# Optimization experiments

Hardware: AMD Instinct MI355X
Metric: run time of the kernel (lower is better)

The kernel has to match this reference:

```python
import jax, jax.numpy as jnp
import numpy as np

B, N, D = 8, 2048, 128
NEG = -9.0e15


def setup_inputs() -> dict:
    key = jax.random.key(0)
    ks = jax.random.split(key, 7)
    x = jax.random.normal(ks[0], (B, N, D), dtype=jnp.float32)
    # sparse-ish binary adjacency with self loops, stored dense as float
    adj = (jax.random.uniform(ks[1], (B, N, N)) < 0.1).astype(jnp.float32)
    adj = jnp.maximum(adj, jnp.eye(N, dtype=jnp.float32)[None])
    s = 1.0 / np.sqrt(D)
    W_w = jax.random.uniform(ks[2], (D, D), minval=-s, maxval=s, dtype=jnp.float32)
    W_b = jax.random.uniform(ks[3], (D,), minval=-s, maxval=s, dtype=jnp.float32)
    A = jnp.zeros((D, D), dtype=jnp.float32) + 0.01 * jax.random.normal(ks[4], (D, D), dtype=jnp.float32)
    s2 = 1.0 / np.sqrt(2 * D)
    gate_w = jax.random.uniform(ks[5], (1, 2 * D), minval=-s2, maxval=s2, dtype=jnp.float32)
    gate_b = jax.random.uniform(ks[6], (1,), minval=-s2, maxval=s2, dtype=jnp.float32)
    return {"x": x, "adj": adj, "W_w": W_w, "W_b": W_b, "A": A,
            "gate_w": gate_w, "gate_b": gate_b}


def reference(x, adj, W_w, W_b, A, gate_w, gate_b):
    # h = W(x): [B,N,D]
    h = jnp.einsum('bnf,df->bnd', x, W_w) + W_b
    # e[b,j,k] = (h A)[b,j,:] . h[b,k,:], then symmetrize
    hA = jnp.einsum('bnd,de->bne', h, A)
    e = jnp.einsum('bjl,bkl->bjk', hA, h)
    e = e + jnp.swapaxes(e, 1, 2)
    att = jnp.where(adj > 0, e, jnp.full_like(e, NEG))
    # NOTE: torch code softmaxes over dim=1 (the j axis)
    att = jax.nn.softmax(att, axis=1)
    att = att * adj
    h_prime = jax.nn.relu(jnp.einsum('bij,bjk->bik', att, h))
    gate_in = jnp.concatenate([x, h_prime], axis=-1)  # [B,N,2D]
    coeff = jax.nn.sigmoid(jnp.einsum('bnc,oc->bno', gate_in, gate_w) + gate_b)  # [B,N,1]
    return coeff * x + (1.0 - coeff) * h_prime
```

## Files before the change

kernel.cpp:

```cpp
#include <hip/hip_runtime.h>


#define B_ 8
#define N_ 2048
#define D_ 128

typedef __attribute__((ext_vector_type(8))) short short8;
typedef __attribute__((ext_vector_type(4))) float f32x4;
typedef __attribute__((ext_vector_type(2))) float f32x2;

#define GLL(gp, lp) __builtin_amdgcn_global_load_lds( \
    (__attribute__((address_space(1))) const unsigned int*)(gp), \
    (__attribute__((address_space(3))) unsigned int*)(lp), 16, 0, 0)

#define VMW(N) asm volatile("s_waitcnt vmcnt(" #N ")" ::: "memory")
#define BARRIER() __builtin_amdgcn_s_barrier()

static __device__ __forceinline__ unsigned short f2bf(float f) {
  union { float f; unsigned int u; } v; v.f = f;
  unsigned int r = v.u + 0x7fffu + ((v.u >> 16) & 1u);
  return (unsigned short)(r >> 16);
}
static __device__ __forceinline__ float bf2f(unsigned short u) {
  union { unsigned int u; float f; } v; v.u = ((unsigned int)u) << 16;
  return v.f;
}

#define CAT_OFF  ((size_t)0)
#define VT_OFF   ((size_t)8388608)
#define PUN_OFF  ((size_t)12582912)
#define S_OFF    ((size_t)79691776)
#define WB_OFF   ((size_t)79757312)
#define AT_OFF   ((size_t)79790080)

__global__ __launch_bounds__(256) void k_cvt(const float* __restrict__ W,
                                             const float* __restrict__ A,
                                             unsigned short* __restrict__ Wb1,
                                             unsigned short* __restrict__ Abt) {
  int i = blockIdx.x * 256 + threadIdx.x;
  Wb1[i] = f2bf(W[i]);
  Abt[(i & 127) * 128 + (i >> 7)] = f2bf(A[i]);
}

__global__ __launch_bounds__(256) void k1(const float* __restrict__ x,
                                          const unsigned short* __restrict__ Wb1,
                                          const float* __restrict__ Wbias,
                                          const unsigned short* __restrict__ Abt,
                                          unsigned short* __restrict__ cat) {
  __shared__ unsigned short hsm[4][16][136];
  __shared__ unsigned short hasm[4][16][136];
  const int t = threadIdx.x, w = t >> 6, lane = t & 63;
  const int q = lane >> 4, l15 = lane & 15;
  const size_t r0 = (size_t)blockIdx.x * 64 + w * 16;

  f32x4 acc[8];
#pragma unroll
  for (int dg = 0; dg < 8; dg++) acc[dg] = (f32x4){0.f, 0.f, 0.f, 0.f};
#pragma unroll
  for (int k = 0; k < 4; k++) {
    const float* xp = x + (r0 + l15) * 128 + k * 32 + q * 8;
    f32x4 xa = *(const f32x4*)xp;
    f32x4 xb = *(const f32x4*)(xp + 4);
    short8 af;
#pragma unroll
    for (int e = 0; e < 4; e++) { af[e] = (short)f2bf(xa[e]); af[4 + e] = (short)f2bf(xb[e]); }
#pragma unroll
    for (int dg = 0; dg < 8; dg++) {
      short8 bf = *(const short8*)(Wb1 + (dg * 16 + l15) * 128 + k * 32 + q * 8);
      acc[dg] = __builtin_amdgcn_mfma_f32_16x16x32_bf16(af, bf, acc[dg], 0, 0, 0);
    }
  }
#pragma unroll
  for (int dg = 0; dg < 8; dg++) {
    float bias = Wbias[dg * 16 + l15];
#pragma unroll
    for (int r = 0; r < 4; r++)
      hsm[w][q * 4 + r][dg * 16 + l15] = f2bf(acc[dg][r] + bias);
  }
  __syncthreads();
  f32x4 acc2[8];
#pragma unroll
  for (int dg = 0; dg < 8; dg++) acc2[dg] = (f32x4){0.f, 0.f, 0.f, 0.f};
#pragma unroll
  for (int k = 0; k < 4; k++) {
    short8 af = *(short8*)&hsm[w][l15][k * 32 + q * 8];
#pragma unroll
    for (int dg = 0; dg < 8; dg++) {
      short8 bf = *(const short8*)(Abt + (dg * 16 + l15) * 128 + k * 32 + q * 8);
      acc2[dg] = __builtin_amdgcn_mfma_f32_16x16x32_bf16(af, bf, acc2[dg], 0, 0, 0);
    }
  }
#pragma unroll
  for (int dg = 0; dg < 8; dg++)
#pragma unroll
    for (int r = 0; r < 4; r++)
      hasm[w][q * 4 + r][dg * 16 + l15] = f2bf(acc2[dg][r]);
  __syncthreads();
#pragma unroll
  for (int it = 0; it < 8; it++) {
    int idx = it * 64 + lane;
    int row = idx >> 5, c = idx & 31;
    short8 v = (c < 16) ? *(short8*)&hasm[w][row][c * 8]
                        : *(short8*)&hsm[w][row][(c - 16) * 8];
    *(short8*)(cat + ((r0 + row) << 8) + c * 8) = v;
  }
}

__global__ __launch_bounds__(256, 2) void k2(const unsigned short* __restrict__ cat,
                                             const float* __restrict__ adj,
                                             unsigned short* __restrict__ pun,
                                             float* __restrict__ s_out) {
  __shared__ unsigned short cj[2][64 * 256];
  const int t = threadIdx.x, w = t >> 6, lane = t & 63;
  const int q = lane >> 4, l15 = lane & 15;
  const int b = blockIdx.z;
  const int kbase = blockIdx.x * 128;
  const int j0b = blockIdx.y * 512;
  const size_t bN = (size_t)b * N_;
  const unsigned short* catp = cat + (bN << 8);
  const int kc = kbase + w * 32;
  short8 brg[2][8];
#pragma unroll
  for (int p = 0; p < 2; p++) {
    int krow = kc + 2 * l15 + p;
#pragma unroll
    for (int m = 0; m < 8; m++)
      brg[p][m] = *(const short8*)(catp + (((size_t)krow) << 8) +
                                   ((((m * 4 + q) + 16) & 31) * 8));
  }
  float acc0 = 0.f, acc1 = 0.f;

#define K2_STAGE(tt, bufi) do { \
    const int j0_ = j0b + (tt) * 64; \
    _Pragma("unroll") \
    for (int it = 0; it < 8; it++) { \
      int sI = it * 256 + t; \
      int row = sI >> 5, c = sI & 31; \
      GLL(catp + (((size_t)(j0_ + row)) << 8) + (c ^ (row & 7)) * 8, \
          (char*)cj[bufi] + sI * 16); \
    } } while (0)

#define K2_ADJ(tt, av) do { \
    const int j0_ = j0b + (tt) * 64; \
    _Pragma("unroll") \
    for (int js = 0; js < 4; js++) \
      _Pragma("unroll") \
      for (int r = 0; r < 4; r++) { \
        int jrow = j0_ + js * 16 + q * 4 + r; \
        av[js][r] = *(const f32x2*)(adj + (((size_t)(bN + jrow)) << 11) + kc + 2 * l15); \
      } } while (0)

#define K2_COMPUTE(tt, bufi, av) do { \
    const int j0_ = j0b + (tt) * 64; \
    _Pragma("unroll") \
    for (int jsub = 0; jsub < 4; jsub++) { \
      const int row = jsub * 16 + l15; \
      short8 afr[8]; \
      _Pragma("unroll") \
      for (int m = 0; m < 8; m++) \
        afr[m] = *(short8*)(cj[bufi] + row * 256 + (((m * 4 + q) ^ (l15 & 7)) * 8)); \
      f32x4 e0 = {0.f, 0.f, 0.f, 0.f}, e1 = {0.f, 0.f, 0.f, 0.f}; \
      _Pragma("unroll") \
      for (int m = 0; m < 8; m++) { \
        e0 = __builtin_amdgcn_mfma_f32_16x16x32_bf16(afr[m], brg[0][m], e0, 0, 0, 0); \
        e1 = __builtin_amdgcn_mfma_f32_16x16x32_bf16(afr[m], brg[1][m], e1, 0, 0, 0); \
      } \
      _Pragma("unroll") \
      for (int r = 0; r < 4; r++) { \
        int jrow = j0_ + jsub * 16 + q * 4 + r; \
        float x0 = (av[jsub][r][0] > 0.f) ? __expf(fminf(e0[r], 60.f)) : 0.f; \
        float x1 = (av[jsub][r][1] > 0.f) ? __expf(fminf(e1[r], 60.f)) : 0.f; \
        acc0 += x0; acc1 += x1; \
        unsigned int pk = (unsigned int)f2bf(x0) | ((unsigned int)f2bf(x1) << 16); \
        *(unsigned int*)(pun + ((bN + jrow) << 11) + kc + 2 * l15) = pk; \
      } \
    } } while (0)

  f32x2 avA[4][4], avB[4][4];
  K2_STAGE(0, 0);
  K2_ADJ(0, avA);
#pragma unroll
  for (int tp = 0; tp < 4; tp++) {
    K2_STAGE(2 * tp + 1, 1);
    K2_ADJ(2 * tp + 1, avB);
    VMW(40);
    BARRIER();
    K2_COMPUTE(2 * tp, 0, avA);
    BARRIER();
    if (2 * tp + 2 < 8) {
      K2_STAGE(2 * tp + 2, 0);
      K2_ADJ(2 * tp + 2, avA);
      VMW(40);
    } else {
      VMW(16);
    }
    BARRIER();
    K2_COMPUTE(2 * tp + 1, 1, avB);
    BARRIER();
  }
#undef K2_STAGE
#undef K2_ADJ
#undef K2_COMPUTE

  acc0 += __shfl_xor(acc0, 16, 64); acc0 += __shfl_xor(acc0, 32, 64);
  acc1 += __shfl_xor(acc1, 16, 64); acc1 += __shfl_xor(acc1, 32, 64);
  if (lane < 16) {
    atomicAdd(&s_out[bN + kc + 2 * lane], acc0);
    atomicAdd(&s_out[bN + kc + 2 * lane + 1], acc1);
  }
}

__global__ __launch_bounds__(256) void k1v(const unsigned short* __restrict__ cat,
                                           const float* __restrict__ s,
                                           unsigned short* __restrict__ vt) {
  __shared__ unsigned short tile[64][136];
  __shared__ float rsv[64];
  const int t = threadIdx.x;
  const int b = blockIdx.y;
  const int nbase = blockIdx.x * 64;
  if (t < 64) rsv[t] = 1.f / s[(size_t)b * N_ + nbase + t];
#pragma unroll
  for (int k = 0; k < 4; k++) {
    int sI = t + 256 * k;
    int row = sI >> 4, part = sI & 15;
    *(short8*)&tile[row][part * 8] =
        *(const short8*)(cat + (((size_t)(b * N_ + nbase + row)) << 8) + 128 + part * 8);
  }
  __syncthreads();
#pragma unroll
  for (int k = 0; k < 4; k++) {
    int sI = t + 256 * k;
    int dd = sI >> 3, part = sI & 7;
    unsigned short tmp[8];
#pragma unroll
    for (int j = 0; j < 8; j++) {
      int jj = part * 8 + j;
      tmp[j] = f2bf(bf2f(tile[jj][dd]) * rsv[jj]);
    }
    *(short8*)(vt + (((size_t)(b * 128 + dd)) << 11) + nbase + part * 8) = *(short8*)tmp;
  }
}

__global__ __launch_bounds__(256) void k3(const unsigned short* __restrict__ pun,
                                          const unsigned short* __restrict__ vt,
                                          const float* __restrict__ x,
                                          const float* __restrict__ gw,
                                          const float* __restrict__ gb,
                                          float* __restrict__ out) {
  __shared__ char smem[2][40960];
  const int t = threadIdx.x, w = t >> 6, lane = t & 63;
  const int q = lane >> 4, l15 = lane & 15;
  const int b = blockIdx.y, i0 = blockIdx.x * 32;
  const size_t bN = (size_t)b * N_;

  f32x4 acc[2][2];
#pragma unroll
  for (int ih = 0; ih < 2; ih++)
#pragma unroll
    for (int dh = 0; dh < 2; dh++) acc[ih][dh] = (f32x4){0.f, 0.f, 0.f, 0.f};

#define K3_STAGE(jtv, bufi) do { \
    const int j0_ = (jtv) * 128; \
    _Pragma("unroll") \
    for (int it = 0; it < 10; it++) { \
      int sI = it * 256 + t; \
      const unsigned short* g; \
      if (sI < 512) { \
        int row = sI >> 4, c = sI & 15; \
        g = pun + (((size_t)(bN + i0 + row)) << 11) + j0_ + ((c ^ (row & 7)) * 8); \
      } else { \
        int s2 = sI - 512; \
        int dd = s2 >> 4, c = s2 & 15; \
        g = vt + (((size_t)(b * 128 + dd)) << 11) + j0_ + ((c ^ (dd & 7)) * 8); \
      } \
      GLL(g, smem[bufi] + sI * 16); \
    } } while (0)

#define K3_COMPUTE(bufi) do { \
    unsigned short* pa = (unsigned short*)smem[bufi]; \
    unsigned short* vb = (unsigned short*)(smem[bufi] + 8192); \
    _Pragma("unroll") \
    for (int ks = 0; ks < 4; ks++) { \
      short8 af[2], bf[2]; \
      _Pragma("unroll") \
      for (int ih = 0; ih < 2; ih++) { \
        int m = ih * 16 + l15; \
        af[ih] = *(short8*)(pa + m * 128 + (((ks * 4 + q) ^ (m & 7)) * 8)); \
      } \
      _Pragma("unroll") \
      for (int dh = 0; dh < 2; dh++) { \
        int d = w * 32 + dh * 16 + l15; \
        bf[dh] = *(short8*)(vb + d * 128 + (((ks * 4 + q) ^ (d & 7)) * 8)); \
      } \
      acc[0][0] = __builtin_amdgcn_mfma_f32_16x16x32_bf16(af[0], bf[0], acc[0][0], 0, 0, 0); \
      acc[0][1] = __builtin_amdgcn_mfma_f32_16x16x32_bf16(af[0], bf[1], acc[0][1], 0, 0, 0); \
      acc[1][0] = __builtin_amdgcn_mfma_f32_16x16x32_bf16(af[1], bf[0], acc[1][0], 0, 0, 0); \
      acc[1][1] = __builtin_amdgcn_mfma_f32_16x16x32_bf16(af[1], bf[1], acc[1][1], 0, 0, 0); \
    } } while (0)

  K3_STAGE(0, 0);
  for (int jt = 0; jt < 15; jt++) {
    K3_STAGE(jt + 1, (jt + 1) & 1);
    asm volatile("s_waitcnt vmcnt(10)" ::: "memory");
    BARRIER();
    K3_COMPUTE(jt & 1);
    BARRIER();
  }
  asm volatile("s_waitcnt vmcnt(0)" ::: "memory");
  BARRIER();
  K3_COMPUTE(1);
  __syncthreads();
#undef K3_STAGE
#undef K3_COMPUTE

  float* hs = (float*)smem[0];
  float* co = (float*)(smem[0] + 16896);
#pragma unroll
  for (int ih = 0; ih < 2; ih++)
#pragma unroll
    for (int dh = 0; dh < 2; dh++)
#pragma unroll
      for (int r = 0; r < 4; r++) {
        int row = ih * 16 + q * 4 + r;
        int d = w * 32 + dh * 16 + l15;
        hs[row * 132 + d] = fmaxf(acc[ih][dh][r], 0.f);
      }
  __syncthreads();
  {
    int grow = t >> 3, sub = t & 7;
    const float* xr = x + (((size_t)(bN + i0 + grow)) << 7);
    float z = 0.f;
#pragma unroll
    for (int k = 0; k < 16; k++) {
      int dd = sub + 8 * k;
      z += gw[dd] * xr[dd] + gw[128 + dd] * hs[grow * 132 + dd];
    }
    z += __shfl_xor(z, 1, 64);
    z += __shfl_xor(z, 2, 64);
    z += __shfl_xor(z, 4, 64);
    if (sub == 0) co[grow] = 1.f / (1.f + __expf(-(z + gb[0])));
  }
  __syncthreads();
#pragma unroll
  for (int kk = 0; kk < 4; kk++) {
    int id = kk * 256 + t;
    int row = id >> 5, c4 = id & 31;
    size_t g = (((size_t)(bN + i0 + row)) << 7) + c4 * 4;
    f32x4 xv = *(const f32x4*)(x + g);
    f32x4 hv = *(const f32x4*)(hs + row * 132 + c4 * 4);
    float cf = co[row];
    f32x4 o;
#pragma unroll
    for (int e = 0; e < 4; e++) o[e] = cf * xv[e] + (1.f - cf) * hv[e];
    *(f32x4*)(out + g) = o;
  }
}

extern "C" void kernel_launch(void* const* d_in, const int* in_sizes, int n_in,
                              void* d_out, int out_size, void* d_ws, size_t ws_size,
                              hipStream_t stream) {
  const float* x   = (const float*)d_in[0];
  const float* adj = (const float*)d_in[1];
  const float* Ww  = (const float*)d_in[2];
  const float* Wb  = (const float*)d_in[3];
  const float* A   = (const float*)d_in[4];
  const float* gw  = (const float*)d_in[5];
  const float* gb  = (const float*)d_in[6];
  float* out = (float*)d_out;
  char* ws = (char*)d_ws;

  unsigned short* cat = (unsigned short*)(ws + CAT_OFF);
  unsigned short* vt  = (unsigned short*)(ws + VT_OFF);
  unsigned short* pun = (unsigned short*)(ws + PUN_OFF);
  float* s  = (float*)(ws + S_OFF);
  unsigned short* Wb1 = (unsigned short*)(ws + WB_OFF);
  unsigned short* Abt = (unsigned short*)(ws + AT_OFF);

  hipMemsetAsync(s, 0, (size_t)B_ * N_ * sizeof(float), stream);
  k_cvt<<<64, 256, 0, stream>>>(Ww, A, Wb1, Abt);
  k1<<<(B_ * N_) / 64, 256, 0, stream>>>(x, Wb1, Wb, Abt, cat);
  k2<<<dim3(16, 4, B_), 256, 0, stream>>>(cat, adj, pun, s);
  k1v<<<dim3(N_ / 64, B_), 256, 0, stream>>>(cat, s, vt);
  k3<<<dim3(N_ / 32, B_), 256, 0, stream>>>(pun, vt, x, gw, gb, out);
}
```

Baseline: 266.3 us.

## Stage adjacency tiles into LDS via async global_load_lds with smaller j tiles

```diff
diff --git a/kernel.cpp b/kernel.cpp
--- a/kernel.cpp
+++ b/kernel.cpp
@@ -110,7 +110,8 @@
                                              const float* __restrict__ adj,
                                              unsigned short* __restrict__ pun,
                                              float* __restrict__ s_out) {
-  __shared__ unsigned short cj[2][64 * 256];
+  __shared__ unsigned short cj[2][32 * 256];
+  __shared__ float aj[2][32 * 128];
   const int t = threadIdx.x, w = t >> 6, lane = t & 63;
   const int q = lane >> 4, l15 = lane & 15;
   const int b = blockIdx.z;
@@ -131,29 +132,26 @@
   float acc0 = 0.f, acc1 = 0.f;
 
 #define K2_STAGE(tt, bufi) do { \
-    const int j0_ = j0b + (tt) * 64; \
-    _Pragma("unroll") \
-    for (int it = 0; it < 8; it++) { \
+    const int j0_ = j0b + (tt) * 32; \
+    _Pragma("unroll") \
+    for (int it = 0; it < 4; it++) { \
       int sI = it * 256 + t; \
       int row = sI >> 5, c = sI & 31; \
       GLL(catp + (((size_t)(j0_ + row)) << 8) + (c ^ (row & 7)) * 8, \
           (char*)cj[bufi] + sI * 16); \
+    } \
+    _Pragma("unroll") \
+    for (int it = 0; it < 4; it++) { \
+      int sI = it * 256 + t; \
+      int row = sI >> 5, c = sI & 31; \
+      GLL(adj + (((size_t)(bN + j0_ + row)) << 11) + kbase + ((c ^ (row & 7)) << 2), \
+          (char*)aj[bufi] + sI * 16); \
     } } while (0)
 
-#define K2_ADJ(tt, av) do { \
-    const int j0_ = j0b + (tt) * 64; \
-    _Pragma("unroll") \
-    for (int js = 0; js < 4; js++) \
-      _Pragma("unroll") \
-      for (int r = 0; r < 4; r++) { \
-        int jrow = j0_ + js * 16 + q * 4 + r; \
-        av[js][r] = *(const f32x2*)(adj + (((size_t)(bN + jrow)) << 11) + kc + 2 * l15); \
-      } } while (0)
-
-#define K2_COMPUTE(tt, bufi, av) do { \
-    const int j0_ = j0b + (tt) * 64; \
-    _Pragma("unroll") \
-    for (int jsub = 0; jsub < 4; jsub++) { \
+#define K2_COMPUTE(tt, bufi) do { \
+    const int j0_ = j0b + (tt) * 32; \
+    _Pragma("unroll") \
+    for (int jsub = 0; jsub < 2; jsub++) { \
       const int row = jsub * 16 + l15; \
       short8 afr[8]; \
       _Pragma("unroll") \
@@ -167,39 +165,36 @@
       } \
       _Pragma("unroll") \
       for (int r = 0; r < 4; r++) { \
-        int jrow = j0_ + jsub * 16 + q * 4 + r; \
-        float x0 = (av[jsub][r][0] > 0.f) ? __expf(fminf(e0[r], 60.f)) : 0.f; \
-        float x1 = (av[jsub][r][1] > 0.f) ? __expf(fminf(e1[r], 60.f)) : 0.f; \
+        int jr = jsub * 16 + q * 4 + r; \
+        int jrow = j0_ + jr; \
+        f32x2 av = *(const f32x2*)((const char*)aj[bufi] + jr * 512 + \
+                    (((w * 8 + (l15 >> 1)) ^ (jr & 7)) << 4) + ((l15 & 1) << 3)); \
+        float x0 = (av[0] > 0.f) ? __expf(fminf(e0[r], 60.f)) : 0.f; \
+        float x1 = (av[1] > 0.f) ? __expf(fminf(e1[r], 60.f)) : 0.f; \
         acc0 += x0; acc1 += x1; \
         unsigned int pk = (unsigned int)f2bf(x0) | ((unsigned int)f2bf(x1) << 16); \
         *(unsigned int*)(pun + ((bN + jrow) << 11) + kc + 2 * l15) = pk; \
       } \
     } } while (0)
 
-  f32x2 avA[4][4], avB[4][4];
   K2_STAGE(0, 0);
-  K2_ADJ(0, avA);
-#pragma unroll
-  for (int tp = 0; tp < 4; tp++) {
-    K2_STAGE(2 * tp + 1, 1);
-    K2_ADJ(2 * tp + 1, avB);
-    VMW(40);
+  K2_STAGE(1, 1);
+  VMW(8);
+  BARRIER();
+  K2_COMPUTE(0, 0);
+  BARRIER();
+#pragma unroll
+  for (int tp = 1; tp < 15; tp++) {
+    K2_STAGE(tp + 1, (tp + 1) & 1);
+    VMW(16);
     BARRIER();
-    K2_COMPUTE(2 * tp, 0, avA);
+    K2_COMPUTE(tp, tp & 1);
     BARRIER();
-    if (2 * tp + 2 < 8) {
-      K2_STAGE(2 * tp + 2, 0);
-      K2_ADJ(2 * tp + 2, avA);
-      VMW(40);
-    } else {
-      VMW(16);
-    }
-    BARRIER();
-    K2_COMPUTE(2 * tp + 1, 1, avB);
-    BARRIER();
-  }
+  }
+  VMW(8);
+  BARRIER();
+  K2_COMPUTE(15, 1);
 #undef K2_STAGE
-#undef K2_ADJ
 #undef K2_COMPUTE
 
   acc0 += __shfl_xor(acc0, 16, 64); acc0 += __shfl_xor(acc0, 32, 64);
```

New measurement: 263.7 us. About the same (-1.0%).
